# Kernel tuning notes

Measured on AMD Instinct MI355X. Metric: run time of the kernel, lower is better.

The kernel has to match this reference:

```python
import math
import jax, jax.numpy as jnp
import numpy as np

HEADS = 8
DIM_HEAD = 64
N_WIN = 6


def setup_inputs() -> dict:
    key = jax.random.key(0)
    ks = jax.random.split(key, 5)
    b, N, D = 1, 12288, 512
    inner = HEADS * DIM_HEAD  # 512
    x = jax.random.normal(ks[0], (b, N, D), dtype=jnp.float32)
    s = 1.0 / math.sqrt(D)
    Wq = jax.random.normal(ks[1], (inner, D), dtype=jnp.float32) * s
    Wk = jax.random.normal(ks[2], (inner, D), dtype=jnp.float32) * s
    Wv = jax.random.normal(ks[3], (inner, D), dtype=jnp.float32) * s
    Wo = jax.random.normal(ks[4], (D, inner), dtype=jnp.float32) * s
    bo = jnp.zeros((D,), dtype=jnp.float32)
    return {"x": x, "Wq": Wq, "Wk": Wk, "Wv": Wv, "Wo": Wo, "bo": bo}


def reference(x, Wq, Wk, Wv, Wo, bo):
    b, N, D = x.shape
    H = int(math.sqrt(N // 12))  # feature map is H x 12H
    W = N // H                   # 12H
    Ww = W // N_WIN              # window width 2H
    L = H * Ww                   # tokens per window

    # projections (torch Linear: y = x @ W^T)
    q = x @ Wq.T
    k = x @ Wk.T
    v = x @ Wv.T

    def to_windows(t):
        # [b, (H W), inner] -> [b, nwin, L, heads, dim_head]; tokens within a
        # window keep (h w) row-major order, matching the torch rearranges.
        t = t.reshape(b, H, N_WIN, Ww, HEADS, DIM_HEAD)
        return t.transpose(0, 2, 1, 3, 4, 5).reshape(b, N_WIN, L, HEADS, DIM_HEAD)

    qw, kw, vw = to_windows(q), to_windows(k), to_windows(v)

    scale = 1.0 / math.sqrt(DIM_HEAD)
    scores = jnp.einsum('bgqhd,bgkhd->bghqk', qw, kw) * scale  # [b,6,h,L,L]
    attn = jax.nn.softmax(scores, axis=-1)
    out = jnp.einsum('bghqk,bgkhd->bgqhd', attn, vw)           # [b,6,L,h,d]

    # windows -> full map -> tokens
    out = out.reshape(b, N_WIN, H, Ww, HEADS * DIM_HEAD)
    out = out.transpose(0, 2, 1, 3, 4).reshape(b, N, HEADS * DIM_HEAD)
    return out @ Wo.T + bo
```

## Files before the change

### kernel.cpp

```cpp
#include <hip/hip_runtime.h>
#include <hip/hip_bf16.h>

typedef __bf16 bf16_t;
typedef __attribute__((ext_vector_type(8))) __bf16 bf16x8;
typedef __attribute__((ext_vector_type(4))) __bf16 bf16x4;
typedef __attribute__((ext_vector_type(4))) float f32x4;

#define MFMA16(a, b, c) __builtin_amdgcn_mfma_f32_16x16x32_bf16((a), (b), (c), 0, 0, 0)
#define EXP2F(x) __builtin_amdgcn_exp2f(x)

#define NTOK 12288
#define DMODEL 512
#define LWIN 2048
#define NGH 48
#define LOG2E 1.44269504088896340736f

__device__ __forceinline__ void async_copy16(const bf16_t* g, bf16_t* l) {
    __builtin_amdgcn_global_load_lds((const __attribute__((address_space(1))) void*)g,
                                     (__attribute__((address_space(3))) void*)l, 16, 0, 0);
}

__global__ void convert_bf16(const float* __restrict__ x,
                             const float* __restrict__ wq, const float* __restrict__ wk,
                             const float* __restrict__ wv, const float* __restrict__ wo,
                             bf16_t* __restrict__ xbf, bf16_t* __restrict__ wqkv,
                             bf16_t* __restrict__ wob2) {
    const int NX = NTOK * DMODEL;
    const int NW = DMODEL * DMODEL;
    const int total4 = (NX + 4 * NW) >> 2;
    for (int i4 = blockIdx.x * blockDim.x + threadIdx.x; i4 < total4;
         i4 += gridDim.x * blockDim.x) {
        int i = i4 << 2;
        if (i < NX + 3 * NW) {
            const float* src; bf16_t* dst; int off;
            if (i < NX)               { src = x;  dst = xbf;           off = i; }
            else if (i < NX + NW)     { src = wq; dst = wqkv;          off = i - NX; }
            else if (i < NX + 2 * NW) { src = wk; dst = wqkv + NW;     off = i - NX - NW; }
            else                      { src = wv; dst = wqkv + 2 * NW; off = i - NX - 2 * NW; }
            float4 v = *reinterpret_cast<const float4*>(src + off);
            bf16x4 o;
            o[0] = (bf16_t)v.x; o[1] = (bf16_t)v.y; o[2] = (bf16_t)v.z; o[3] = (bf16_t)v.w;
            *reinterpret_cast<bf16x4*>(dst + off) = o;
        } else {
            int off = i - NX - 3 * NW;
            int j = off >> 9, k = off & 511;
            float4 v = *reinterpret_cast<const float4*>(wo + off);
            bf16x4 hi, lo;
            float f[4] = {v.x, v.y, v.z, v.w};
#pragma unroll
            for (int t = 0; t < 4; t++) {
                bf16_t h = (bf16_t)f[t];
                hi[t] = h;
                lo[t] = (bf16_t)(f[t] - (float)h);
            }
            *reinterpret_cast<bf16x4*>(wob2 + (size_t)j * 1024 + k) = hi;
            *reinterpret_cast<bf16x4*>(wob2 + (size_t)j * 1024 + 512 + k) = lo;
        }
    }
}

__global__ __launch_bounds__(256, 2) void gemm_qkv(
    const bf16_t* __restrict__ A, const bf16_t* __restrict__ B,
    bf16_t* __restrict__ qw, bf16_t* __restrict__ kw, bf16_t* __restrict__ vtw) {
    __shared__ __align__(16) bf16_t smem[2 * 128 * 64];
    bf16_t* sA = smem;
    bf16_t* sB = smem + 128 * 64;
    const int tm = blockIdx.x / 12, tn = blockIdx.x % 12;
    const int tid = threadIdx.x;
    const int lane = tid & 63, wid = tid >> 6;
    const int llo = lane & 15, lhi = lane >> 4;
    const int wr = wid >> 1, wc = wid & 1;

    f32x4 acc[4][4];
    const f32x4 zero = {0.f, 0.f, 0.f, 0.f};
#pragma unroll
    for (int i = 0; i < 4; i++)
#pragma unroll
        for (int j = 0; j < 4; j++) acc[i][j] = zero;

    const bf16_t* Ab = A + (size_t)(tm * 128) * DMODEL;
    const bf16_t* Bb = B + (size_t)(tn * 128) * DMODEL;

    for (int k0 = 0; k0 < DMODEL; k0 += 64) {
#pragma unroll
        for (int s = 0; s < 4; s++) {
            int chunk = tid + s * 256;
            int row = chunk >> 3, c8 = chunk & 7;
            async_copy16(Ab + (size_t)row * DMODEL + k0 + c8 * 8, sA + chunk * 8);
            async_copy16(Bb + (size_t)row * DMODEL + k0 + c8 * 8, sB + chunk * 8);
        }
        __syncthreads();
#pragma unroll
        for (int kk = 0; kk < 2; kk++) {
            bf16x8 af[4], bfr[4];
#pragma unroll
            for (int mi = 0; mi < 4; mi++)
                af[mi] = *reinterpret_cast<const bf16x8*>(
                    &sA[(wr * 64 + mi * 16 + llo) * 64 + kk * 32 + lhi * 8]);
#pragma unroll
            for (int ni = 0; ni < 4; ni++)
                bfr[ni] = *reinterpret_cast<const bf16x8*>(
                    &sB[(wc * 64 + ni * 16 + llo) * 64 + kk * 32 + lhi * 8]);
#pragma unroll
            for (int mi = 0; mi < 4; mi++)
#pragma unroll
                for (int ni = 0; ni < 4; ni++)
                    acc[mi][ni] = MFMA16(af[mi], bfr[ni], acc[mi][ni]);
        }
        __syncthreads();
    }

    const int row0 = tm * 128 + wr * 64;
    const int col0 = tn * 128 + wc * 64;
    if (tn < 8) {
#pragma unroll
        for (int mi = 0; mi < 4; mi++) {
#pragma unroll
            for (int ni = 0; ni < 4; ni++) {
                int j = col0 + ni * 16 + llo;
                int which = j >> 9;
                int head = (j >> 6) & 7;
                int dim = j & 63;
#pragma unroll
                for (int r = 0; r < 4; r++) {
                    int n = row0 + mi * 16 + lhi * 4 + r;
                    float val = acc[mi][ni][r];
                    int hr = n / 384;
                    int rem = n - hr * 384;
                    int g = rem >> 6, w = rem & 63;
                    int l = (hr << 6) + w;
                    size_t gh = (size_t)(g * 8 + head);
                    if (which == 0)
                        qw[(gh * LWIN + l) * 64 + dim] = (bf16_t)(val * (0.125f * LOG2E));
                    else
                        kw[(gh * LWIN + l) * 64 + dim] = (bf16_t)val;
                }
            }
        }
    } else {
        bf16_t* vt = smem;
#pragma unroll
        for (int half = 0; half < 2; half++) {
            if (wr == half) {
#pragma unroll
                for (int mi = 0; mi < 4; mi++)
#pragma unroll
                    for (int ni = 0; ni < 4; ni++) {
                        int col_local = wc * 64 + ni * 16 + llo;
#pragma unroll
                        for (int r = 0; r < 4; r++) {
                            int row_local = mi * 16 + lhi * 4 + r;
                            vt[col_local * 72 + row_local] = (bf16_t)acc[mi][ni][r];
                        }
                    }
            }
            __syncthreads();
            int n0 = tm * 128 + half * 64;
            int hr = n0 / 384;
            int g = (n0 - hr * 384) >> 6;
#pragma unroll
            for (int p = 0; p < 4; p++) {
                int drow = p * 32 + (tid >> 3);
                int lch = (tid & 7) * 8;
                bf16x8 vv = *reinterpret_cast<const bf16x8*>(&vt[drow * 72 + lch]);
                int jj = (tn - 8) * 128 + drow;
                int head = jj >> 6, dim = jj & 63;
                size_t R = (size_t)(g * 8 + head) * 64 + dim;
                *reinterpret_cast<bf16x8*>(&vtw[R * LWIN + hr * 64 + lch]) = vv;
            }
            __syncthreads();
        }
    }
}

__global__ __launch_bounds__(256, 4) void attn_win(
    const bf16_t* __restrict__ qw, const bf16_t* __restrict__ kw,
    const bf16_t* __restrict__ vtw, bf16_t* __restrict__ aout2) {
    __shared__ __align__(16) bf16_t sK[2][64 * 64];
    __shared__ __align__(16) bf16_t sV[2][64 * 64];
    __shared__ __align__(16) bf16_t P[4][16 * 64];

    const int b = blockIdx.x;
    const int xcd = b & 7;
    const int slot = b >> 3;
    const int gh = xcd * 6 + (slot >> 4);
    const int qtile = slot & 15;
    const int g = gh >> 3, h = gh & 7;
    const int tid = threadIdx.x, lane = tid & 63, wid = tid >> 6;
    const int llo = lane & 15, lhi = lane >> 4;

    const bf16_t* Qb = qw + (size_t)gh * LWIN * 64;
    const bf16_t* Kb = kw + (size_t)gh * LWIN * 64;
    const bf16_t* Vb = vtw + (size_t)gh * 64 * LWIN;

    const int q0 = qtile * 128;
    bf16x8 qa[2][2];
#pragma unroll
    for (int qf = 0; qf < 2; qf++)
#pragma unroll
        for (int dk = 0; dk < 2; dk++)
            qa[qf][dk] = *reinterpret_cast<const bf16x8*>(
                &Qb[(size_t)(q0 + qf * 64 + wid * 16 + llo) * 64 + dk * 32 + lhi * 8]);

    f32x4 O[2][4];
    float rs[2][4];
    const f32x4 zero = {0.f, 0.f, 0.f, 0.f};
#pragma unroll
    for (int qf = 0; qf < 2; qf++) {
#pragma unroll
        for (int dc = 0; dc < 4; dc++) O[qf][dc] = zero;
#pragma unroll
        for (int r = 0; r < 4; r++) rs[qf][r] = 0.f;
    }

    auto stage = [&](int buf, int k0) {
#pragma unroll
        for (int s = 0; s < 2; s++) {
            int chunk = tid + s * 256;
            int row = chunk >> 3, c8 = chunk & 7;
            int c8g = c8 ^ (row & 7);
            async_copy16(Kb + (size_t)(k0 + row) * 64 + c8g * 8,
                         &sK[buf][chunk * 8]);
            async_copy16(Vb + (size_t)row * LWIN + k0 + c8g * 8,
                         &sV[buf][chunk * 8]);
        }
    };

    stage(0, 0);
    __syncthreads();

#pragma unroll 2
    for (int t = 0; t < 32; t++) {
        const int cur = t & 1;
        if (t < 31) stage(cur ^ 1, (t + 1) * 64);

        bf16x8 bk[4][2];
#pragma unroll
        for (int kc = 0; kc < 4; kc++) {
            int row = kc * 16 + llo;
#pragma unroll
            for (int kk = 0; kk < 2; kk++)
                bk[kc][kk] = *reinterpret_cast<const bf16x8*>(
                    &sK[cur][row * 64 + (((kk * 4 + lhi) ^ (row & 7)) * 8)]);
        }

        bf16x8 pa[2][2];
#pragma unroll
        for (int qf = 0; qf < 2; qf++) {
            f32x4 s4[4];
            __builtin_amdgcn_s_setprio(1);
#pragma unroll
            for (int kc = 0; kc < 4; kc++) {
                f32x4 acc = zero;
                acc = MFMA16(qa[qf][0], bk[kc][0], acc);
                acc = MFMA16(qa[qf][1], bk[kc][1], acc);
                s4[kc] = acc;
            }
            __builtin_amdgcn_s_setprio(0);
#pragma unroll
            for (int kc = 0; kc < 4; kc++)
#pragma unroll
                for (int r = 0; r < 4; r++) {
                    float p = EXP2F(s4[kc][r]);
                    rs[qf][r] += p;
                    int row = lhi * 4 + r;
                    int chn = (kc * 2 + (llo >> 3)) ^ (row & 7);
                    P[wid][row * 64 + chn * 8 + (llo & 7)] = (bf16_t)p;
                }
#pragma unroll
            for (int ks = 0; ks < 2; ks++)
                pa[qf][ks] = *reinterpret_cast<const bf16x8*>(
                    &P[wid][llo * 64 + (((ks * 4 + lhi) ^ (llo & 7)) * 8)]);
        }

        __builtin_amdgcn_s_setprio(1);
#pragma unroll
        for (int dc = 0; dc < 4; dc++) {
            int row = dc * 16 + llo;
            bf16x8 bv0 = *reinterpret_cast<const bf16x8*>(
                &sV[cur][row * 64 + (((0 + lhi) ^ (row & 7)) * 8)]);
            bf16x8 bv1 = *reinterpret_cast<const bf16x8*>(
                &sV[cur][row * 64 + (((4 + lhi) ^ (row & 7)) * 8)]);
#pragma unroll
            for (int qf = 0; qf < 2; qf++) {
                O[qf][dc] = MFMA16(pa[qf][0], bv0, O[qf][dc]);
                O[qf][dc] = MFMA16(pa[qf][1], bv1, O[qf][dc]);
            }
        }
        __builtin_amdgcn_s_setprio(0);
        __syncthreads();
    }

#pragma unroll
    for (int qf = 0; qf < 2; qf++)
#pragma unroll
        for (int r = 0; r < 4; r++) {
            float t = rs[qf][r];
#pragma unroll
            for (int off = 1; off < 16; off <<= 1) t += __shfl_xor(t, off, 64);
            rs[qf][r] = 1.0f / t;
        }
#pragma unroll
    for (int qf = 0; qf < 2; qf++)
#pragma unroll
        for (int dc = 0; dc < 4; dc++)
#pragma unroll
            for (int r = 0; r < 4; r++) {
                int l = q0 + qf * 64 + wid * 16 + lhi * 4 + r;
                int hr = l >> 6, w = l & 63;
                int n = hr * 384 + g * 64 + w;
                float o = O[qf][dc][r] * rs[qf][r];
                bf16_t hv = (bf16_t)o;
                size_t base = (size_t)n * 1024 + h * 64 + dc * 16 + llo;
                aout2[base] = hv;
                aout2[base + 512] = (bf16_t)(o - (float)hv);
            }
}

__global__ __launch_bounds__(256, 2) void gemm_out(
    const bf16_t* __restrict__ A2, const bf16_t* __restrict__ B2,
    const float* __restrict__ bias, float* __restrict__ C) {
    __shared__ __align__(16) bf16_t sA[128 * 64];
    __shared__ __align__(16) bf16_t sB[64 * 64];
    const int tm = blockIdx.x >> 3, tn = blockIdx.x & 7;
    const int tid = threadIdx.x;
    const int lane = tid & 63, wid = tid >> 6;
    const int llo = lane & 15, lhi = lane >> 4;
    const int wr = wid >> 1, wc = wid & 1;

    f32x4 acc[4][2];
    const f32x4 zero = {0.f, 0.f, 0.f, 0.f};
#pragma unroll
    for (int i = 0; i < 4; i++)
#pragma unroll
        for (int j = 0; j < 2; j++) acc[i][j] = zero;

    const bf16_t* Ab = A2 + (size_t)(tm * 128) * 1024;
    const bf16_t* Bb = B2 + (size_t)(tn * 64) * 1024;

    for (int k0 = 0; k0 < 1536; k0 += 64) {
        const int kb = k0 >> 9;
        const int ka = k0 & 511;
        const int kA = (kb == 1 ? 512 : 0) + ka;
        const int kB = (kb == 2 ? 512 : 0) + ka;
#pragma unroll
        for (int s = 0; s < 4; s++) {
            int chunk = tid + s * 256;
            int row = chunk >> 3, c8 = chunk & 7;
            async_copy16(Ab + (size_t)row * 1024 + kA + c8 * 8, sA + chunk * 8);
        }
#pragma unroll
        for (int s = 0; s < 2; s++) {
            int chunk = tid + s * 256;
            int row = chunk >> 3, c8 = chunk & 7;
            async_copy16(Bb + (size_t)row * 1024 + kB + c8 * 8, sB + chunk * 8);
        }
        __syncthreads();
#pragma unroll
        for (int kk = 0; kk < 2; kk++) {
            bf16x8 af[4], bfr[2];
#pragma unroll
            for (int mi = 0; mi < 4; mi++)
                af[mi] = *reinterpret_cast<const bf16x8*>(
                    &sA[(wr * 64 + mi * 16 + llo) * 64 + kk * 32 + lhi * 8]);
#pragma unroll
            for (int ni = 0; ni < 2; ni++)
                bfr[ni] = *reinterpret_cast<const bf16x8*>(
                    &sB[(wc * 32 + ni * 16 + llo) * 64 + kk * 32 + lhi * 8]);
#pragma unroll
            for (int mi = 0; mi < 4; mi++)
#pragma unroll
                for (int ni = 0; ni < 2; ni++)
                    acc[mi][ni] = MFMA16(af[mi], bfr[ni], acc[mi][ni]);
        }
        __syncthreads();
    }

    const int row0 = tm * 128 + wr * 64;
    const int col0 = tn * 64 + wc * 32;
#pragma unroll
    for (int mi = 0; mi < 4; mi++) {
#pragma unroll
        for (int ni = 0; ni < 2; ni++) {
            int j = col0 + ni * 16 + llo;
            float bv = bias[j];
#pragma unroll
            for (int r = 0; r < 4; r++) {
                int n = row0 + mi * 16 + lhi * 4 + r;
                C[(size_t)n * DMODEL + j] = acc[mi][ni][r] + bv;
            }
        }
    }
}

extern "C" void kernel_launch(void* const* d_in, const int* in_sizes, int n_in,
                              void* d_out, int out_size, void* d_ws, size_t ws_size,
                              hipStream_t stream) {
    const float* x  = (const float*)d_in[0];
    const float* Wq = (const float*)d_in[1];
    const float* Wk = (const float*)d_in[2];
    const float* Wv = (const float*)d_in[3];
    const float* Wo = (const float*)d_in[4];
    const float* bo = (const float*)d_in[5];
    float* out = (float*)d_out;

    const size_t NX = (size_t)NTOK * DMODEL;
    const size_t NW = (size_t)DMODEL * DMODEL;
    bf16_t* xbf   = (bf16_t*)d_ws;
    bf16_t* wqkv  = xbf + NX;
    bf16_t* wob2  = wqkv + 3 * NW;
    bf16_t* qw    = wob2 + 2 * NW;
    bf16_t* kw    = qw + NX;
    bf16_t* vtw   = kw + NX;
    bf16_t* aout2 = vtw + NX;

    convert_bf16<<<2048, 256, 0, stream>>>(x, Wq, Wk, Wv, Wo, xbf, wqkv, wob2);

    gemm_qkv<<<96 * 12, 256, 0, stream>>>(xbf, wqkv, qw, kw, vtw);

    attn_win<<<768, 256, 0, stream>>>(qw, kw, vtw, aout2);

    gemm_out<<<96 * 8, 256, 0, stream>>>(aout2, wob2, bo, out);
}
```

Before: 353.6 us.

## Store attention output in fp32 and split to bf16 hi/lo inside output GEMM

```diff
diff --git a/kernel.cpp b/kernel.cpp
--- a/kernel.cpp
+++ b/kernel.cpp
@@ -175,9 +175,8 @@
 
 __global__ __launch_bounds__(256, 4) void attn_win(
     const bf16_t* __restrict__ qw, const bf16_t* __restrict__ kw,
-    const bf16_t* __restrict__ vtw, bf16_t* __restrict__ aout2) {
-    __shared__ __align__(16) bf16_t sK[2][64 * 64];
-    __shared__ __align__(16) bf16_t sV[2][64 * 64];
+    const bf16_t* __restrict__ vtw, float* __restrict__ aout) {
+    __shared__ __align__(16) bf16_t sKV[4][64 * 64];
     __shared__ __align__(16) bf16_t P[4][16 * 64];
 
     const int b = blockIdx.x;
@@ -220,9 +219,9 @@
             int row = chunk >> 3, c8 = chunk & 7;
             int c8g = c8 ^ (row & 7);
             async_copy16(Kb + (size_t)(k0 + row) * 64 + c8g * 8,
-                         &sK[buf][chunk * 8]);
+                         &sKV[buf][chunk * 8]);
             async_copy16(Vb + (size_t)row * LWIN + k0 + c8g * 8,
-                         &sV[buf][chunk * 8]);
+                         &sKV[2 + buf][chunk * 8]);
         }
     };
 
@@ -241,7 +240,7 @@
 #pragma unroll
             for (int kk = 0; kk < 2; kk++)
                 bk[kc][kk] = *reinterpret_cast<const bf16x8*>(
-                    &sK[cur][row * 64 + (((kk * 4 + lhi) ^ (row & 7)) * 8)]);
+                    &sKV[cur][row * 64 + (((kk * 4 + lhi) ^ (row & 7)) * 8)]);
         }
 
         bf16x8 pa[2][2];
@@ -278,9 +277,9 @@
         for (int dc = 0; dc < 4; dc++) {
             int row = dc * 16 + llo;
             bf16x8 bv0 = *reinterpret_cast<const bf16x8*>(
-                &sV[cur][row * 64 + (((0 + lhi) ^ (row & 7)) * 8)]);
+                &sKV[2 + cur][row * 64 + (((0 + lhi) ^ (row & 7)) * 8)]);
             bf16x8 bv1 = *reinterpret_cast<const bf16x8*>(
-                &sV[cur][row * 64 + (((4 + lhi) ^ (row & 7)) * 8)]);
+                &sKV[2 + cur][row * 64 + (((4 + lhi) ^ (row & 7)) * 8)]);
 #pragma unroll
             for (int qf = 0; qf < 2; qf++) {
                 O[qf][dc] = MFMA16(pa[qf][0], bv0, O[qf][dc]);
@@ -309,79 +308,80 @@
                 int l = q0 + qf * 64 + wid * 16 + lhi * 4 + r;
                 int hr = l >> 6, w = l & 63;
                 int n = hr * 384 + g * 64 + w;
-                float o = O[qf][dc][r] * rs[qf][r];
-                bf16_t hv = (bf16_t)o;
-                size_t base = (size_t)n * 1024 + h * 64 + dc * 16 + llo;
-                aout2[base] = hv;
-                aout2[base + 512] = (bf16_t)(o - (float)hv);
+                aout[(size_t)n * DMODEL + h * 64 + dc * 16 + llo] =
+                    O[qf][dc][r] * rs[qf][r];
             }
 }
 
 __global__ __launch_bounds__(256, 2) void gemm_out(
-    const bf16_t* __restrict__ A2, const bf16_t* __restrict__ B2,
+    const float* __restrict__ A, const bf16_t* __restrict__ B2,
     const float* __restrict__ bias, float* __restrict__ C) {
     __shared__ __align__(16) bf16_t sA[128 * 64];
-    __shared__ __align__(16) bf16_t sB[64 * 64];
-    const int tm = blockIdx.x >> 3, tn = blockIdx.x & 7;
+    __shared__ __align__(16) bf16_t sB[128 * 64];
+    const int tm = blockIdx.x >> 2, tn = blockIdx.x & 3;
     const int tid = threadIdx.x;
     const int lane = tid & 63, wid = tid >> 6;
     const int llo = lane & 15, lhi = lane >> 4;
     const int wr = wid >> 1, wc = wid & 1;
 
-    f32x4 acc[4][2];
+    f32x4 acc[4][4];
     const f32x4 zero = {0.f, 0.f, 0.f, 0.f};
 #pragma unroll
     for (int i = 0; i < 4; i++)
 #pragma unroll
-        for (int j = 0; j < 2; j++) acc[i][j] = zero;
-
-    const bf16_t* Ab = A2 + (size_t)(tm * 128) * 1024;
-    const bf16_t* Bb = B2 + (size_t)(tn * 64) * 1024;
+        for (int j = 0; j < 4; j++) acc[i][j] = zero;
+
+    const float* Ab = A + (size_t)(tm * 128) * DMODEL;
+    const bf16_t* Bb = B2 + (size_t)(tn * 128) * 1024;
 
     for (int k0 = 0; k0 < 1536; k0 += 64) {
         const int kb = k0 >> 9;
         const int ka = k0 & 511;
-        const int kA = (kb == 1 ? 512 : 0) + ka;
         const int kB = (kb == 2 ? 512 : 0) + ka;
 #pragma unroll
         for (int s = 0; s < 4; s++) {
             int chunk = tid + s * 256;
             int row = chunk >> 3, c8 = chunk & 7;
-            async_copy16(Ab + (size_t)row * 1024 + kA + c8 * 8, sA + chunk * 8);
-        }
-#pragma unroll
-        for (int s = 0; s < 2; s++) {
-            int chunk = tid + s * 256;
-            int row = chunk >> 3, c8 = chunk & 7;
+            const float* ap = Ab + (size_t)row * DMODEL + ka + c8 * 8;
+            float4 f0 = *reinterpret_cast<const float4*>(ap);
+            float4 f1 = *reinterpret_cast<const float4*>(ap + 4);
+            float f[8] = {f0.x, f0.y, f0.z, f0.w, f1.x, f1.y, f1.z, f1.w};
+            bf16x8 o;
+#pragma unroll
+            for (int t = 0; t < 8; t++) {
+                bf16_t hv = (bf16_t)f[t];
+                o[t] = (kb == 1) ? (bf16_t)(f[t] - (float)hv) : hv;
+            }
+            *reinterpret_cast<bf16x8*>(&sA[chunk * 8]) = o;
             async_copy16(Bb + (size_t)row * 1024 + kB + c8 * 8, sB + chunk * 8);
         }
         __syncthreads();
 #pragma unroll
         for (int kk = 0; kk < 2; kk++) {
-            bf16x8 af[4], bfr[2];
+            bf16x8 af[4], bfr[4];
 #pragma unroll
             for (int mi = 0; mi < 4; mi++)
                 af[mi] = *reinterpret_cast<const bf16x8*>(
                     &sA[(wr * 64 + mi * 16 + llo) * 64 + kk * 32 + lhi * 8]);
 #pragma unroll
-            for (int ni = 0; ni < 2; ni++)
+            for (int ni = 0; ni < 4; ni++)
                 bfr[ni] = *reinterpret_cast<const bf16x8*>(
-                    &sB[(wc * 32 + ni * 16 + llo) * 64 + kk * 32 + lhi * 8]);
+                    &sB[(wc * 64 + ni * 16 + llo) * 64 + kk * 32 + lhi * 8]);
 #pragma unroll
             for (int mi = 0; mi < 4; mi++)
 #pragma unroll
-                for (int ni = 0; ni < 2; ni++)
+                for (int ni = 0; ni < 4; ni++)
                     acc[mi][ni] = MFMA16(af[mi], bfr[ni], acc[mi][ni]);
         }
         __syncthreads();
     }
 
     const int row0 = tm * 128 + wr * 64;
-    const int col0 = tn * 64 + wc * 32;
+    const int col0 = tn * 128 + wc * 64;
 #pragma unroll
     for (int mi = 0; mi < 4; mi++) {
 #pragma unroll
-        for (int ni = 0; ni < 2; ni++) {
+        for (int ni = 0; ni < 4; ni++) {
             int j = col0 + ni * 16 + llo;
             float bv = bias[j];
 #pragma unroll
@@ -412,13 +412,13 @@
     bf16_t* qw    = wob2 + 2 * NW;
     bf16_t* kw    = qw + NX;
     bf16_t* vtw   = kw + NX;
-    bf16_t* aout2 = vtw + NX;
+    float*  aoutf = (float*)(vtw + NX);
 
     convert_bf16<<<2048, 256, 0, stream>>>(x, Wq, Wk, Wv, Wo, xbf, wqkv, wob2);
 
     gemm_qkv<<<96 * 12, 256, 0, stream>>>(xbf, wqkv, qw, kw, vtw);
 
-    attn_win<<<768, 256, 0, stream>>>(qw, kw, vtw, aout2);
-
-    gemm_out<<<96 * 8, 256, 0, stream>>>(aout2, wob2, bo, out);
-}
+    attn_win<<<768, 256, 0, stream>>>(qw, kw, vtw, aoutf);
+
+    gemm_out<<<96 * 4, 256, 0, stream>>>(aoutf, wob2, bo, out);
+}
```

New measurement: 425.6 us. 1.2x slower.
